# Performance work log

Measured on AMD Instinct MI355X. Metric: run time of the kernel, lower is better.

The kernel has to match this reference:

```python
import jax, jax.numpy as jnp
import numpy as np

LN_EPS = 1e-5
START_TOKEN = 0  # voc['<s>']

V, E = 512, 512
H = 2 * E            # 1024
B, T = 256, 128


def setup_inputs() -> dict:
    key = jax.random.key(0)
    ks = jax.random.split(key, 12)
    s = lambda *shape: 0.05  # small init scale
    return {
        "target": jax.random.randint(ks[0], (B, T), 0, V),
        "emb": jax.random.normal(ks[1], (V, E), jnp.float32) * 0.05,
        "projW": jax.random.normal(ks[2], (H, E), jnp.float32) * 0.05,
        "projb": jnp.zeros((H,), jnp.float32),
        "gru_Wih": jax.random.normal(ks[3], (3, 3 * H, H), jnp.float32) * 0.03,
        "gru_Whh": jax.random.normal(ks[4], (3, 3 * H, H), jnp.float32) * 0.03,
        "gru_bih": jnp.zeros((3, 3 * H), jnp.float32),
        "gru_bhh": jnp.zeros((3, 3 * H), jnp.float32),
        "ln_s": jnp.ones((3, H), jnp.float32),
        "ln_b": jnp.zeros((3, H), jnp.float32),
        "fc1W": jax.random.normal(ks[5], (2 * H, H), jnp.float32) * 0.03,
        "fc1b": jnp.zeros((2 * H,), jnp.float32),
        "fc2W": jax.random.normal(ks[6], (V, 2 * H), jnp.float32) * 0.03,
        "fc2b": jnp.zeros((V,), jnp.float32),
    }


def _layernorm(x, scale, bias):
    mu = jnp.mean(x, axis=-1, keepdims=True)
    var = jnp.mean(jnp.square(x - mu), axis=-1, keepdims=True)
    return (x - mu) * jax.lax.rsqrt(var + LN_EPS) * scale + bias


def _gru_cell(x, h, Wih, Whh, bih, bhh):
    # PyTorch GRUCell: gates stacked [r; z; n] along dim 0 of [3H, H] weights
    gi = x @ Wih.T + bih      # [B, 3H]
    gh = h @ Whh.T + bhh      # [B, 3H]
    i_r, i_z, i_n = jnp.split(gi, 3, axis=-1)
    h_r, h_z, h_n = jnp.split(gh, 3, axis=-1)
    r = jax.nn.sigmoid(i_r + h_r)
    z = jax.nn.sigmoid(i_z + h_z)
    n = jnp.tanh(i_n + r * h_n)
    return (1.0 - z) * n + z * h


def reference(target, emb, projW, projb, gru_Wih, gru_Whh, gru_bih, gru_bhh,
              ln_s, ln_b, fc1W, fc1b, fc2W, fc2b):
    # teacher-forced likelihood: x_t = [<s>, target_0, ..., target_{T-2}]
    bsz = target.shape[0]
    start = jnp.full((bsz, 1), START_TOKEN, dtype=target.dtype)
    x_in = jnp.concatenate([start, target[:, :-1]], axis=1)   # [B, T]

    def step(carry, xs):
        h, acc = carry                 # h: [3, B, H]
        tok, tgt = xs                  # [B], [B]
        x = emb[tok]                   # [B, E]  embedding gather
        x = x @ projW.T + projb        # [B, H]  (dropout = identity in eval)
        new_h = []
        for i in range(3):             # three structurally distinct cells
            hi = _gru_cell(x, h[i], gru_Wih[i], gru_Whh[i], gru_bih[i], gru_bhh[i])
            hi = _layernorm(hi + x, ln_s[i], ln_b[i])
            new_h.append(hi)
            x = hi
        logits = jax.nn.relu(x @ fc1W.T + fc1b) @ fc2W.T + fc2b   # [B, V]
        lp = jax.nn.log_softmax(logits, axis=-1)
        acc = acc + jnp.take_along_axis(lp, tgt[:, None], axis=1)[:, 0]
        return (jnp.stack(new_h, axis=0), acc), None

    h0 = jnp.zeros((3, bsz, projW.shape[0]), dtype=projW.dtype)
    acc0 = jnp.zeros((bsz,), dtype=projW.dtype)
    (_, log_probs), _ = jax.lax.scan(step, (h0, acc0), (x_in.T, target.T))
    return log_probs
```

## Files before the change

kernel.cpp:

```cpp
#include <hip/hip_runtime.h>
#include <stdint.h>

#define HID   1024
#define B3H   3072
#define BSZ   256
#define TLEN  128
#define VOC   512
#define EMB   512
#define SLAB  ((size_t)BSZ * B3H)

typedef unsigned short u16;
typedef short bf16x8 __attribute__((ext_vector_type(8)));
typedef float f32x4  __attribute__((ext_vector_type(4)));

__device__ __forceinline__ float bf2f(u16 u) {
    union { float f; uint32_t i; } c; c.i = ((uint32_t)u) << 16; return c.f;
}
__device__ __forceinline__ u16 f2bf(float f) {
    union { float f; uint32_t i; } c; c.f = f;
    uint32_t u = c.i;
    return (u16)((u + 0x7FFFu + ((u >> 16) & 1u)) >> 16);
}
__device__ __forceinline__ float sigm(float x)  { return 1.f / (1.f + __expf(-x)); }
__device__ __forceinline__ float tanhf_(float x) {
    float e = __expf(-2.f * fabsf(x));
    float r = (1.f - e) / (1.f + e);
    return x < 0.f ? -r : r;
}

__device__ __forceinline__ void gll16(const u16* g, u16* l) {
    __builtin_amdgcn_global_load_lds(
        (__attribute__((address_space(1))) void*)(u16*)g,
        (__attribute__((address_space(3))) void*)l, 16, 0, 0);
}

__device__ __forceinline__ void stage_tile(const u16* __restrict__ src, int ld,
                                           u16* __restrict__ lds, int wid, int lane) {
#pragma unroll
    for (int i = 0; i < 2; i++) {
        int row16 = wid * 2 + i;
        const u16* g = src + (size_t)(row16 * 16 + (lane >> 2)) * ld + (lane & 3) * 8;
        u16* l = lds + row16 * 16 * 32;
        gll16(g, l);
    }
}

template<int KTOT>
__device__ __forceinline__ void gemm_tiles(const u16* __restrict__ A, const u16* __restrict__ W,
                                           f32x4 acc[4][4], int wid, int lane) {
    __shared__ u16 As[2][128 * 32], Ws[2][128 * 32];
    const int r = lane & 15, g8 = (lane >> 4) * 8;
    const int mq = wid & 1, nq = wid >> 1;
    int buf = 0;
    stage_tile(A, KTOT, As[0], wid, lane);
    stage_tile(W, KTOT, Ws[0], wid, lane);
    __syncthreads();
    for (int k0 = 0; k0 < KTOT; k0 += 32) {
        if (k0 + 32 < KTOT) {
            stage_tile(A + k0 + 32, KTOT, As[buf ^ 1], wid, lane);
            stage_tile(W + k0 + 32, KTOT, Ws[buf ^ 1], wid, lane);
        }
        bf16x8 a[4], b[4];
#pragma unroll
        for (int i = 0; i < 4; i++) a[i] = *(const bf16x8*)(As[buf] + (mq * 64 + i * 16 + r) * 32 + g8);
#pragma unroll
        for (int i = 0; i < 4; i++) b[i] = *(const bf16x8*)(Ws[buf] + (nq * 64 + i * 16 + r) * 32 + g8);
#pragma unroll
        for (int mi = 0; mi < 4; mi++)
#pragma unroll
            for (int ni = 0; ni < 4; ni++)
                acc[mi][ni] = __builtin_amdgcn_mfma_f32_16x16x32_bf16(a[mi], b[ni], acc[mi][ni], 0, 0, 0);
        __syncthreads();
        buf ^= 1;
    }
}

__global__ void k_convert(const float* __restrict__ in, u16* __restrict__ out, int n) {
    int i = (blockIdx.x * 256 + threadIdx.x) * 4;
    if (i >= n) return;
    float4 f = *(const float4*)(in + i);
    uint32_t lo = (uint32_t)f2bf(f.x) | ((uint32_t)f2bf(f.y) << 16);
    uint32_t hi = (uint32_t)f2bf(f.z) | ((uint32_t)f2bf(f.w) << 16);
    uint2 p; p.x = lo; p.y = hi;
    *(uint2*)(out + i) = p;
}

__global__ void __launch_bounds__(256) k_proj(const u16* __restrict__ emb_bf, const u16* __restrict__ projW_bf,
                       const float* __restrict__ projb, const int* __restrict__ target,
                       u16* __restrict__ X_all) {
    int tn = blockIdx.x * 64, tm = blockIdx.y * 64;
    int wid = threadIdx.x >> 6, lane = threadIdx.x & 63;
    int rr = lane & 15, g = lane >> 4;
    int rowg = tm + wid * 16 + rr;
    int t = rowg >> 8, b = rowg & 255;
    int tok = (t == 0) ? 0 : target[b * TLEN + t - 1];
    const u16* ap = emb_bf + (size_t)tok * EMB + g * 8;
    f32x4 acc[4];
#pragma unroll
    for (int n = 0; n < 4; n++) for (int q = 0; q < 4; q++) acc[n][q] = 0.f;
#pragma unroll 4
    for (int k = 0; k < EMB; k += 32) {
        bf16x8 a = *(const bf16x8*)(ap + k);
#pragma unroll
        for (int n = 0; n < 4; n++) {
            bf16x8 bb = *(const bf16x8*)(projW_bf + (size_t)(tn + n * 16 + rr) * EMB + g * 8 + k);
            acc[n] = __builtin_amdgcn_mfma_f32_16x16x32_bf16(a, bb, acc[n], 0, 0, 0);
        }
    }
    int c = lane & 15, r0 = (lane >> 4) * 4;
    u16* Cw = X_all + (size_t)(tm + wid * 16) * HID + tn;
#pragma unroll
    for (int n = 0; n < 4; n++)
#pragma unroll
        for (int q = 0; q < 4; q++)
            Cw[(size_t)(r0 + q) * HID + n * 16 + c] = f2bf(acc[n][q] + projb[tn + n * 16 + c]);
}

__global__ void __launch_bounds__(256) k_gstep(int wv,
    const u16* __restrict__ X_all, const u16* __restrict__ h_bf,
    const u16* __restrict__ Wih, const u16* __restrict__ Whh,
    float* __restrict__ giP, float* __restrict__ ghP) {
    int bid = blockIdx.x;
    int g = bid / 48, rem = bid % 48, mt = rem / 24, nt = rem % 24;
    int cell = g % 3; bool isgh = (g >= 3);
    int t = wv - cell;
    if (t < 0 || t >= TLEN) return;
    int rd = (wv + 1) & 1;
    const u16* A;
    if (isgh)            A = h_bf + (size_t)(rd * 3 + cell)     * BSZ * HID;
    else if (cell == 0)  A = X_all + (size_t)t * BSZ * HID;
    else                 A = h_bf + (size_t)(rd * 3 + cell - 1) * BSZ * HID;
    A += (size_t)(mt * 128) * HID;
    const u16* W = (isgh ? Whh : Wih) + (size_t)cell * B3H * HID + (size_t)(nt * 128) * HID;
    float*     C = (isgh ? ghP : giP) + (size_t)cell * SLAB + (size_t)(mt * 128) * B3H + nt * 128;

    int wid = threadIdx.x >> 6, lane = threadIdx.x & 63;
    f32x4 acc[4][4] = {};
    gemm_tiles<HID>(A, W, acc, wid, lane);
    int mq = wid & 1, nq = wid >> 1;
    int c = lane & 15, r0 = (lane >> 4) * 4;
#pragma unroll
    for (int mi = 0; mi < 4; mi++)
#pragma unroll
        for (int e = 0; e < 4; e++) {
            float* Cw = C + (size_t)(mq * 64 + mi * 16 + r0 + e) * B3H;
#pragma unroll
            for (int ni = 0; ni < 4; ni++)
                Cw[nq * 64 + ni * 16 + c] = acc[mi][ni][e];
        }
}

template<int KTOT, int EPI>
__global__ void __launch_bounds__(256) k_gemm_s(const u16* __restrict__ A, const u16* __restrict__ W,
                                                const float* __restrict__ bias, void* __restrict__ Cout, int ldc) {
    int nt = blockIdx.x, mt = blockIdx.y;
    int wid = threadIdx.x >> 6, lane = threadIdx.x & 63;
    f32x4 acc[4][4] = {};
    gemm_tiles<KTOT>(A + (size_t)(mt * 128) * KTOT, W + (size_t)(nt * 128) * KTOT, acc, wid, lane);
    int mq = wid & 1, nq = wid >> 1;
    int c = lane & 15, r0 = (lane >> 4) * 4;
#pragma unroll
    for (int mi = 0; mi < 4; mi++)
#pragma unroll
        for (int e = 0; e < 4; e++) {
            size_t row = (size_t)(mt * 128 + mq * 64 + mi * 16 + r0 + e);
#pragma unroll
            for (int ni = 0; ni < 4; ni++) {
                int col = nt * 128 + nq * 64 + ni * 16 + c;
                float x = acc[mi][ni][e] + bias[col];
                if (EPI == 1) ((u16*)Cout)[row * ldc + col] = f2bf(fmaxf(x, 0.f));
                else          ((float*)Cout)[row * ldc + col] = x;
            }
        }
}

__global__ void __launch_bounds__(256) k_wew(int wv,
    const float* __restrict__ giP, const float* __restrict__ ghP,
    const float* __restrict__ bih_all, const float* __restrict__ bhh_all,
    float* __restrict__ h_f32, u16* __restrict__ h_bf, u16* __restrict__ X_all,
    const float* __restrict__ ln_s_all, const float* __restrict__ ln_b_all) {
    int cell = blockIdx.y;
    int t = wv - cell;
    if (t < 0 || t >= TLEN) return;
    int wid = threadIdx.x >> 6, lane = threadIdx.x & 63;
    int b = blockIdx.x * 4 + wid;
    int rd = (wv + 1) & 1, wr = wv & 1;

    const float* gi  = giP + (size_t)cell * SLAB + (size_t)b * B3H;
    const float* gh  = ghP + (size_t)cell * SLAB + (size_t)b * B3H;
    const float* bih = bih_all + cell * B3H;
    const float* bhh = bhh_all + cell * B3H;
    const float* lns = ln_s_all + cell * HID;
    const float* lnb = ln_b_all + cell * HID;
    const float* hprev = h_f32 + ((size_t)(rd * 3 + cell) * BSZ + b) * HID;
    float*       hout  = h_f32 + ((size_t)(wr * 3 + cell) * BSZ + b) * HID;
    u16*         hbout = h_bf  + ((size_t)(wr * 3 + cell) * BSZ + b) * HID;
    const float* xsrcf = (cell > 0) ? h_f32 + ((size_t)(rd * 3 + cell - 1) * BSZ + b) * HID : nullptr;
    const u16*   xsrcb = X_all + ((size_t)t * BSZ + b) * HID;

    float val[16], s = 0.f, s2 = 0.f;
#pragma unroll
    for (int e = 0; e < 4; e++) {
        int j = e * 256 + lane * 4;
        float gg[3][4], hh[3][4];
#pragma unroll
        for (int g = 0; g < 3; g++) {
            int o = g * HID + j;
            f32x4 a = __builtin_nontemporal_load((const f32x4*)(gi + o));
            float4 ab = *(const float4*)(bih + o);
            gg[g][0] = a[0] + ab.x; gg[g][1] = a[1] + ab.y; gg[g][2] = a[2] + ab.z; gg[g][3] = a[3] + ab.w;
            f32x4 h4 = __builtin_nontemporal_load((const f32x4*)(gh + o));
            float4 hb = *(const float4*)(bhh + o);
            hh[g][0] = h4[0] + hb.x; hh[g][1] = h4[1] + hb.y; hh[g][2] = h4[2] + hb.z; hh[g][3] = h4[3] + hb.w;
        }
        float4 hp = *(const float4*)(hprev + j);
        float hpv[4] = {hp.x, hp.y, hp.z, hp.w};
        float xv[4];
        if (cell == 0) {
            ushort4 u = *(const ushort4*)(xsrcb + j);
            xv[0] = bf2f(u.x); xv[1] = bf2f(u.y); xv[2] = bf2f(u.z); xv[3] = bf2f(u.w);
        } else {
            float4 x4 = *(const float4*)(xsrcf + j);
            xv[0] = x4.x; xv[1] = x4.y; xv[2] = x4.z; xv[3] = x4.w;
        }
#pragma unroll
        for (int q = 0; q < 4; q++) {
            float r = sigm(gg[0][q] + hh[0][q]);
            float z = sigm(gg[1][q] + hh[1][q]);
            float n = tanhf_(gg[2][q] + r * hh[2][q]);
            float v = (1.f - z) * n + z * hpv[q] + xv[q];
            val[e * 4 + q] = v; s += v; s2 += v * v;
        }
    }
#pragma unroll
    for (int o = 32; o > 0; o >>= 1) { s += __shfl_xor(s, o); s2 += __shfl_xor(s2, o); }
    float mu = s * (1.f / HID);
    float inv = rsqrtf(s2 * (1.f / HID) - mu * mu + 1e-5f);
#pragma unroll
    for (int e = 0; e < 4; e++) {
        int j = e * 256 + lane * 4;
        float4 sc = *(const float4*)(lns + j);
        float4 bi = *(const float4*)(lnb + j);
        float o0 = (val[e * 4 + 0] - mu) * inv * sc.x + bi.x;
        float o1 = (val[e * 4 + 1] - mu) * inv * sc.y + bi.y;
        float o2 = (val[e * 4 + 2] - mu) * inv * sc.z + bi.z;
        float o3 = (val[e * 4 + 3] - mu) * inv * sc.w + bi.w;
        float4 of; of.x = o0; of.y = o1; of.z = o2; of.w = o3;
        *(float4*)(hout + j) = of;
        u16 b0 = f2bf(o0), b1 = f2bf(o1), b2 = f2bf(o2), b3 = f2bf(o3);
        uint64_t packed = (uint64_t)b0 | ((uint64_t)b1 << 16) | ((uint64_t)b2 << 32) | ((uint64_t)b3 << 48);
        *(uint64_t*)(hbout + j) = packed;
        if (cell == 2) {
            __builtin_nontemporal_store(packed, (uint64_t*)(X_all + ((size_t)t * BSZ + b) * HID + j));
        }
    }
}

__global__ void __launch_bounds__(256) k_lse2(const float* __restrict__ part, const int* __restrict__ target,
                       int c0, float* __restrict__ LP) {
    int wid = threadIdx.x >> 6, lane = threadIdx.x & 63;
    int r = blockIdx.x * 4 + wid;
    const float* row = part + (size_t)r * VOC;
    float v[8];
#pragma unroll
    for (int e = 0; e < 8; e++) v[e] = row[e * 64 + lane];
    float m = v[0];
#pragma unroll
    for (int e = 1; e < 8; e++) m = fmaxf(m, v[e]);
    for (int o = 32; o > 0; o >>= 1) m = fmaxf(m, __shfl_xor(m, o));
    float s = 0.f;
#pragma unroll
    for (int e = 0; e < 8; e++) s += __expf(v[e] - m);
    for (int o = 32; o > 0; o >>= 1) s += __shfl_xor(s, o);
    int t = c0 + (r >> 8), b = r & 255;
    int tg = target[b * TLEN + t];
    float tv = 0.f;
#pragma unroll
    for (int e = 0; e < 8; e++) if (e * 64 + lane == tg) tv = v[e];
    for (int o = 32; o > 0; o >>= 1) tv += __shfl_xor(tv, o);
    if (lane == 0) LP[(size_t)t * BSZ + b] = tv - (m + logf(s));
}

__global__ void k_out(const float* __restrict__ LP, float* __restrict__ out) {
    int b = threadIdx.x;
    float s = 0.f;
    for (int t = 0; t < TLEN; t++) s += LP[(size_t)t * BSZ + b];
    out[b] = s;
}

extern "C" void kernel_launch(void* const* d_in, const int* in_sizes, int n_in,
                              void* d_out, int out_size, void* d_ws, size_t ws_size,
                              hipStream_t stream) {
    const int*   target = (const int*)  d_in[0];
    const float* emb    = (const float*)d_in[1];
    const float* projW  = (const float*)d_in[2];
    const float* projb  = (const float*)d_in[3];
    const float* gWih   = (const float*)d_in[4];
    const float* gWhh   = (const float*)d_in[5];
    const float* gbih   = (const float*)d_in[6];
    const float* gbhh   = (const float*)d_in[7];
    const float* ln_s   = (const float*)d_in[8];
    const float* ln_b   = (const float*)d_in[9];
    const float* fc1W   = (const float*)d_in[10];
    const float* fc1b   = (const float*)d_in[11];
    const float* fc2W   = (const float*)d_in[12];
    const float* fc2b   = (const float*)d_in[13];
    float* out = (float*)d_out;

    char* ws = (char*)d_ws;
    size_t off = 0;
    auto alloc = [&](size_t bytes) { void* p = ws + off; off += (bytes + 511) & ~511ull; return p; };
    u16* emb_bf   = (u16*)alloc((size_t)VOC * EMB * 2);
    u16* projW_bf = (u16*)alloc((size_t)HID * EMB * 2);
    u16* Wih_bf   = (u16*)alloc((size_t)3 * B3H * HID * 2);
    u16* Whh_bf   = (u16*)alloc((size_t)3 * B3H * HID * 2);
    u16* X_all    = (u16*)alloc((size_t)TLEN * BSZ * HID * 2);
    float* h_f32  = (float*)alloc((size_t)2 * 3 * BSZ * HID * 4);
    u16*   h_bf   = (u16*)alloc((size_t)2 * 3 * BSZ * HID * 2);
    float* LP     = (float*)alloc((size_t)TLEN * BSZ * 4);
    float* giP    = (float*)alloc(3 * SLAB * 4);
    float* ghP    = (float*)alloc(3 * SLAB * 4);
    if (off > ws_size) return;

    u16*   fc1W_bf = (u16*)giP;
    u16*   fc2W_bf = (u16*)((char*)giP + (size_t)2048 * HID * 2);
    u16*   a1c     = (u16*)ghP;
    float* partc   = (float*)h_f32;

    auto cvt = [&](const float* s, u16* d, int n) {
        k_convert<<<dim3((n / 4 + 255) / 256), 256, 0, stream>>>(s, d, n);
    };
    cvt(emb,   emb_bf,   VOC * EMB);
    cvt(projW, projW_bf, HID * EMB);
    cvt(gWih,  Wih_bf,   3 * B3H * HID);
    cvt(gWhh,  Whh_bf,   3 * B3H * HID);
    (void)hipMemsetAsync(h_f32, 0, (size_t)2 * 3 * BSZ * HID * 4, stream);
    (void)hipMemsetAsync(h_bf,  0, (size_t)2 * 3 * BSZ * HID * 2, stream);

    k_proj<<<dim3(HID / 64, (TLEN * BSZ) / 64), 256, 0, stream>>>(emb_bf, projW_bf, projb, target, X_all);

    for (int wv = 0; wv < TLEN + 2; wv++) {
        k_gstep<<<dim3(288), 256, 0, stream>>>(wv, X_all, h_bf, Wih_bf, Whh_bf, giP, ghP);
        k_wew<<<dim3(BSZ / 4, 3), 256, 0, stream>>>(wv, giP, ghP, gbih, gbhh, h_f32, h_bf, X_all, ln_s, ln_b);
    }

    cvt(fc1W, fc1W_bf, 2048 * HID);
    cvt(fc2W, fc2W_bf, VOC * 2048);
    const int CH = 8;
    for (int c0 = 0; c0 < TLEN; c0 += CH) {
        int M = CH * BSZ;
        const u16* Ain = X_all + (size_t)c0 * BSZ * HID;
        k_gemm_s<HID, 1><<<dim3(2048 / 128, M / 128), 256, 0, stream>>>(Ain, fc1W_bf, fc1b, a1c, 2048);
        k_gemm_s<2048, 2><<<dim3(VOC / 128, M / 128), 256, 0, stream>>>(a1c, fc2W_bf, fc2b, partc, VOC);
        k_lse2<<<dim3(M / 4), 256, 0, stream>>>(partc, target, c0, LP);
    }
    k_out<<<1, 256, 0, stream>>>(LP, out);
}
```

Before: 5.232 ms.

## Halve recurrent GEMM M-tile to double blocks; LDS-staged tiled projection kernel

The per-step gate GEMM kernel now uses 64x128 tiles instead of 128x128, which doubles the grid from 288 to 576 blocks. The goal is better occupancy across the MI355X CUs during the 130 sequential wavefront steps. Separately, the embedding projection is rewritten as a 128x128 LDS double-buffered MFMA GEMM that gathers embedding rows straight into shared memory, replacing direct global loads from registers. Smaller step tiles reduce weight reuse per block and add more weight traffic from L2.

```diff
diff --git a/kernel.cpp b/kernel.cpp
--- a/kernel.cpp
+++ b/kernel.cpp
@@ -43,6 +43,11 @@
         u16* l = lds + row16 * 16 * 32;
         gll16(g, l);
     }
+}
+__device__ __forceinline__ void stage_tile64(const u16* __restrict__ src, int ld,
+                                             u16* __restrict__ lds, int wid, int lane) {
+    const u16* g = src + (size_t)(wid * 16 + (lane >> 2)) * ld + (lane & 3) * 8;
+    gll16(g, lds + wid * 16 * 32);
 }
 
 template<int KTOT>
@@ -75,6 +80,36 @@
     }
 }
 
+template<int KTOT>
+__device__ __forceinline__ void gemm_tiles64(const u16* __restrict__ A, const u16* __restrict__ W,
+                                             f32x4 acc[2][4], int wid, int lane) {
+    __shared__ u16 As[2][64 * 32], Ws[2][128 * 32];
+    const int r = lane & 15, g8 = (lane >> 4) * 8;
+    const int mq = wid & 1, nq = wid >> 1;
+    int buf = 0;
+    stage_tile64(A, KTOT, As[0], wid, lane);
+    stage_tile(W, KTOT, Ws[0], wid, lane);
+    __syncthreads();
+    for (int k0 = 0; k0 < KTOT; k0 += 32) {
+        if (k0 + 32 < KTOT) {
+            stage_tile64(A + k0 + 32, KTOT, As[buf ^ 1], wid, lane);
+            stage_tile(W + k0 + 32, KTOT, Ws[buf ^ 1], wid, lane);
+        }
+        bf16x8 a[2], b[4];
+#pragma unroll
+        for (int i = 0; i < 2; i++) a[i] = *(const bf16x8*)(As[buf] + (mq * 32 + i * 16 + r) * 32 + g8);
+#pragma unroll
+        for (int i = 0; i < 4; i++) b[i] = *(const bf16x8*)(Ws[buf] + (nq * 64 + i * 16 + r) * 32 + g8);
+#pragma unroll
+        for (int mi = 0; mi < 2; mi++)
+#pragma unroll
+            for (int ni = 0; ni < 4; ni++)
+                acc[mi][ni] = __builtin_amdgcn_mfma_f32_16x16x32_bf16(a[mi], b[ni], acc[mi][ni], 0, 0, 0);
+        __syncthreads();
+        buf ^= 1;
+    }
+}
+
 __global__ void k_convert(const float* __restrict__ in, u16* __restrict__ out, int n) {
     int i = (blockIdx.x * 256 + threadIdx.x) * 4;
     if (i >= n) return;
@@ -85,35 +120,61 @@
     *(uint2*)(out + i) = p;
 }
 
-__global__ void __launch_bounds__(256) k_proj(const u16* __restrict__ emb_bf, const u16* __restrict__ projW_bf,
-                       const float* __restrict__ projb, const int* __restrict__ target,
-                       u16* __restrict__ X_all) {
-    int tn = blockIdx.x * 64, tm = blockIdx.y * 64;
+__global__ void __launch_bounds__(256) k_proj_s(const u16* __restrict__ emb_bf, const u16* __restrict__ projW_bf,
+                        const float* __restrict__ projb, const int* __restrict__ target,
+                        u16* __restrict__ X_all) {
+    int nt = blockIdx.x, mt = blockIdx.y;
     int wid = threadIdx.x >> 6, lane = threadIdx.x & 63;
-    int rr = lane & 15, g = lane >> 4;
-    int rowg = tm + wid * 16 + rr;
-    int t = rowg >> 8, b = rowg & 255;
-    int tok = (t == 0) ? 0 : target[b * TLEN + t - 1];
-    const u16* ap = emb_bf + (size_t)tok * EMB + g * 8;
-    f32x4 acc[4];
-#pragma unroll
-    for (int n = 0; n < 4; n++) for (int q = 0; q < 4; q++) acc[n][q] = 0.f;
-#pragma unroll 4
-    for (int k = 0; k < EMB; k += 32) {
-        bf16x8 a = *(const bf16x8*)(ap + k);
-#pragma unroll
-        for (int n = 0; n < 4; n++) {
-            bf16x8 bb = *(const bf16x8*)(projW_bf + (size_t)(tn + n * 16 + rr) * EMB + g * 8 + k);
-            acc[n] = __builtin_amdgcn_mfma_f32_16x16x32_bf16(a, bb, acc[n], 0, 0, 0);
-        }
+    __shared__ u16 As[2][128 * 32], Ws[2][128 * 32];
+    const u16* arow[2];
+#pragma unroll
+    for (int i = 0; i < 2; i++) {
+        int lr = (wid * 2 + i) * 16 + (lane >> 2);
+        int gr = mt * 128 + lr;
+        int t = gr >> 8, b = gr & 255;
+        int tok = (t == 0) ? 0 : target[b * TLEN + t - 1];
+        arow[i] = emb_bf + (size_t)tok * EMB + (lane & 3) * 8;
+    }
+    const u16* W = projW_bf + (size_t)(nt * 128) * EMB;
+    const int r = lane & 15, g8 = (lane >> 4) * 8;
+    const int mq = wid & 1, nq = wid >> 1;
+    f32x4 acc[4][4] = {};
+    int buf = 0;
+#pragma unroll
+    for (int i = 0; i < 2; i++) gll16(arow[i], As[0] + (wid * 2 + i) * 512);
+    stage_tile(W, EMB, Ws[0], wid, lane);
+    __syncthreads();
+    for (int k0 = 0; k0 < EMB; k0 += 32) {
+        if (k0 + 32 < EMB) {
+#pragma unroll
+            for (int i = 0; i < 2; i++) gll16(arow[i] + k0 + 32, As[buf ^ 1] + (wid * 2 + i) * 512);
+            stage_tile(W + k0 + 32, EMB, Ws[buf ^ 1], wid, lane);
+        }
+        bf16x8 a[4], b[4];
+#pragma unroll
+        for (int i = 0; i < 4; i++) a[i] = *(const bf16x8*)(As[buf] + (mq * 64 + i * 16 + r) * 32 + g8);
+#pragma unroll
+        for (int i = 0; i < 4; i++) b[i] = *(const bf16x8*)(Ws[buf] + (nq * 64 + i * 16 + r) * 32 + g8);
+#pragma unroll
+        for (int mi = 0; mi < 4; mi++)
+#pragma unroll
+            for (int ni = 0; ni < 4; ni++)
+                acc[mi][ni] = __builtin_amdgcn_mfma_f32_16x16x32_bf16(a[mi], b[ni], acc[mi][ni], 0, 0, 0);
+        __syncthreads();
+        buf ^= 1;
     }
     int c = lane & 15, r0 = (lane >> 4) * 4;
-    u16* Cw = X_all + (size_t)(tm + wid * 16) * HID + tn;
-#pragma unroll
-    for (int n = 0; n < 4; n++)
-#pragma unroll
-        for (int q = 0; q < 4; q++)
-            Cw[(size_t)(r0 + q) * HID + n * 16 + c] = f2bf(acc[n][q] + projb[tn + n * 16 + c]);
+#pragma unroll
+    for (int mi = 0; mi < 4; mi++)
+#pragma unroll
+        for (int e = 0; e < 4; e++) {
+            size_t row = (size_t)(mt * 128 + mq * 64 + mi * 16 + r0 + e);
+#pragma unroll
+            for (int ni = 0; ni < 4; ni++) {
+                int col = nt * 128 + nq * 64 + ni * 16 + c;
+                X_all[row * HID + col] = f2bf(acc[mi][ni][e] + projb[col]);
+            }
+        }
 }
 
 __global__ void __launch_bounds__(256) k_gstep(int wv,
@@ -121,7 +182,7 @@
     const u16* __restrict__ Wih, const u16* __restrict__ Whh,
     float* __restrict__ giP, float* __restrict__ ghP) {
     int bid = blockIdx.x;
-    int g = bid / 48, rem = bid % 48, mt = rem / 24, nt = rem % 24;
+    int g = bid / 96, rem = bid % 96, mt = rem / 24, nt = rem % 24;
     int cell = g % 3; bool isgh = (g >= 3);
     int t = wv - cell;
     if (t < 0 || t >= TLEN) return;
@@ -130,20 +191,20 @@
     if (isgh)            A = h_bf + (size_t)(rd * 3 + cell)     * BSZ * HID;
     else if (cell == 0)  A = X_all + (size_t)t * BSZ * HID;
     else                 A = h_bf + (size_t)(rd * 3 + cell - 1) * BSZ * HID;
-    A += (size_t)(mt * 128) * HID;
+    A += (size_t)(mt * 64) * HID;
     const u16* W = (isgh ? Whh : Wih) + (size_t)cell * B3H * HID + (size_t)(nt * 128) * HID;
-    float*     C = (isgh ? ghP : giP) + (size_t)cell * SLAB + (size_t)(mt * 128) * B3H + nt * 128;
+    float*     C = (isgh ? ghP : giP) + (size_t)cell * SLAB + (size_t)(mt * 64) * B3H + nt * 128;
 
     int wid = threadIdx.x >> 6, lane = threadIdx.x & 63;
-    f32x4 acc[4][4] = {};
-    gemm_tiles<HID>(A, W, acc, wid, lane);
+    f32x4 acc[2][4] = {};
+    gemm_tiles64<HID>(A, W, acc, wid, lane);
     int mq = wid & 1, nq = wid >> 1;
     int c = lane & 15, r0 = (lane >> 4) * 4;
 #pragma unroll
-    for (int mi = 0; mi < 4; mi++)
+    for (int mi = 0; mi < 2; mi++)
 #pragma unroll
         for (int e = 0; e < 4; e++) {
-            float* Cw = C + (size_t)(mq * 64 + mi * 16 + r0 + e) * B3H;
+            float* Cw = C + (size_t)(mq * 32 + mi * 16 + r0 + e) * B3H;
 #pragma unroll
             for (int ni = 0; ni < 4; ni++)
                 Cw[nq * 64 + ni * 16 + c] = acc[mi][ni][e];
@@ -337,10 +398,10 @@
     (void)hipMemsetAsync(h_f32, 0, (size_t)2 * 3 * BSZ * HID * 4, stream);
     (void)hipMemsetAsync(h_bf,  0, (size_t)2 * 3 * BSZ * HID * 2, stream);
 
-    k_proj<<<dim3(HID / 64, (TLEN * BSZ) / 64), 256, 0, stream>>>(emb_bf, projW_bf, projb, target, X_all);
+    k_proj_s<<<dim3(HID / 128, (TLEN * BSZ) / 128), 256, 0, stream>>>(emb_bf, projW_bf, projb, target, X_all);
 
     for (int wv = 0; wv < TLEN + 2; wv++) {
-        k_gstep<<<dim3(288), 256, 0, stream>>>(wv, X_all, h_bf, Wih_bf, Whh_bf, giP, ghP);
+        k_gstep<<<dim3(576), 256, 0, stream>>>(wv, X_all, h_bf, Wih_bf, Whh_bf, giP, ghP);
         k_wew<<<dim3(BSZ / 4, 3), 256, 0, stream>>>(wv, giP, ghP, gbih, gbhh, h_f32, h_bf, X_all, ln_s, ln_b);
     }
 
```

After: 5.563 ms. 6.3% more time.
